# Performance work log

Hardware: AMD Instinct MI355X
Metric: run time of the kernel (lower is better)

Reference implementation:

```python
import jax, jax.numpy as jnp
import numpy as np

B, S, HID = 1, 2048, 4096
H, NOPE, ROPE, VD = 32, 128, 64, 128
QKD = NOPE + ROPE
Q_RANK, KV_RANK = 1536, 512
IDX_H, IDX_D, TOPK = 16, 128, 1024
EPS, THETA = 1e-5, 10000.0


def rmsnorm(x, w):
    return x * jax.lax.rsqrt(jnp.mean(x * x, axis=-1, keepdims=True) + EPS) * w


def rope_interleaved(x, pos):
    # x: [..., s, d]; rope_interleave=True -> rotate adjacent pairs
    d = x.shape[-1]
    inv_freq = 1.0 / (THETA ** (jnp.arange(0, d, 2, dtype=jnp.float32) / d))
    ang = pos[:, None] * inv_freq[None, :]  # [s, d/2]
    cos, sin = jnp.cos(ang), jnp.sin(ang)
    x2 = x.reshape(*x.shape[:-1], d // 2, 2)
    x0, x1 = x2[..., 0], x2[..., 1]
    return jnp.stack([x0 * cos - x1 * sin, x1 * cos + x0 * sin], axis=-1).reshape(x.shape)


def setup_inputs() -> dict:
    key = jax.random.key(0)
    ks = jax.random.split(key, 12)
    s = 0.02
    return {
        'hidden_states': jax.random.normal(ks[0], (B, S, HID), jnp.float32),
        'q_a_w': jax.random.normal(ks[1], (HID, Q_RANK), jnp.float32) * s,
        'q_a_norm_w': jnp.ones((Q_RANK,), jnp.float32),
        'q_b_w': jax.random.normal(ks[2], (Q_RANK, H * QKD), jnp.float32) * s,
        'kv_a_w': jax.random.normal(ks[3], (HID, KV_RANK + ROPE), jnp.float32) * s,
        'kv_a_norm_w': jnp.ones((KV_RANK,), jnp.float32),
        'kv_b_w': jax.random.normal(ks[4], (KV_RANK, H * (NOPE + VD)), jnp.float32) * s,
        'o_w': jax.random.normal(ks[5], (H * VD, HID), jnp.float32) * s,
        'idx_wq_w': jax.random.normal(ks[6], (HID, IDX_H * IDX_D), jnp.float32) * s,
        'idx_wk_w': jax.random.normal(ks[7], (HID, IDX_D), jnp.float32) * s,
        'idx_weights_w': jax.random.normal(ks[8], (HID, IDX_H), jnp.float32) * s,
    }


def reference(hidden_states, q_a_w, q_a_norm_w, q_b_w, kv_a_w, kv_a_norm_w,
              kv_b_w, o_w, idx_wq_w, idx_wk_w, idx_weights_w):
    b, s, _ = hidden_states.shape
    pos = jnp.arange(s, dtype=jnp.float32)

    # ---- MLA latent projections ----
    q_lat = rmsnorm(hidden_states @ q_a_w, q_a_norm_w)                 # [b,s,Q_RANK]
    q = (q_lat @ q_b_w).reshape(b, s, H, QKD).transpose(0, 2, 1, 3)    # [b,h,s,qkd]
    q_nope, q_pe = q[..., :NOPE], q[..., NOPE:]

    ckv = hidden_states @ kv_a_w                                       # [b,s,KV_RANK+ROPE]
    kv_lat, k_pe = ckv[..., :KV_RANK], ckv[..., KV_RANK:]
    kv = (rmsnorm(kv_lat, kv_a_norm_w) @ kv_b_w).reshape(b, s, H, NOPE + VD).transpose(0, 2, 1, 3)
    k_nope, v = kv[..., :NOPE], kv[..., NOPE:]

    q_pe = rope_interleaved(q_pe, pos)
    k_pe = rope_interleaved(k_pe[:, None, :, :], pos)                  # [b,1,s,ROPE] shared MQA rope head

    scores = (jnp.einsum('bhqd,bhkd->bhqk', q_nope, k_nope)
              + jnp.einsum('bhqd,bhkd->bhqk', q_pe, k_pe)) * (QKD ** -0.5)

    # ---- DSA lightning indexer: per-query top-k key selection ----
    iq = (hidden_states @ idx_wq_w).reshape(b, s, IDX_H, IDX_D)
    ik = hidden_states @ idx_wk_w                                      # [b,s,IDX_D]
    iw = (hidden_states @ idx_weights_w) * (IDX_H ** -0.5)             # [b,s,IDX_H]
    idx_scores = jnp.einsum('bqn,bnqk->bqk', iw,
                            jax.nn.relu(jnp.einsum('bqnd,bkd->bnqk', iq, ik))) * (IDX_D ** -0.5)
    causal = pos[:, None] >= pos[None, :]                              # [s,s]
    idx_scores = jnp.where(causal, idx_scores, -jnp.inf)
    _, topk_idx = jax.lax.top_k(idx_scores, TOPK)                      # [b,s,TOPK]
    bi = jnp.arange(b)[:, None, None]
    qi = jnp.arange(s)[None, :, None]
    topk_mask = jnp.zeros((b, s, s), bool).at[bi, qi, topk_idx].set(True)
    mask = topk_mask & causal                                          # [b,s,s]

    scores = jnp.where(mask[:, None], scores, -jnp.inf)
    attn = jax.nn.softmax(scores, axis=-1)
    out = jnp.einsum('bhqk,bhkd->bqhd', attn, v).reshape(b, s, H * VD)
    return out @ o_w
```

## Files before the change

### kernel.cpp

```cpp
#include <hip/hip_runtime.h>
#include <math.h>

#define S_LEN 2048
#define HIDDEN 4096
#define NHEAD 32
#define D_NOPE 128
#define D_ROPE 64
#define D_V 128
#define D_QK 192
#define QRANK 1536
#define KVRANK 512
#define IDXH 16
#define IDXD 128
#define KSEL 1024
#define NIDX 2304

typedef __attribute__((ext_vector_type(8))) short bf16x8;
typedef __attribute__((ext_vector_type(4))) float f32x4;
typedef __attribute__((ext_vector_type(4))) unsigned short u16x4;

__device__ __forceinline__ unsigned short f2b(float f) {
    union { float f; unsigned int u; } x; x.f = f;
    unsigned int r = x.u + 0x7FFFu + ((x.u >> 16) & 1u);
    return (unsigned short)(r >> 16);
}
__device__ __forceinline__ float b2f(unsigned short u) {
    union { unsigned int u; float f; } x; x.u = ((unsigned int)u) << 16; return x.f;
}

__device__ __forceinline__ void gload16(const void* g, const void* l) {
    __builtin_amdgcn_global_load_lds(
        (const __attribute__((address_space(1))) unsigned int*)(unsigned long long)g,
        (__attribute__((address_space(3))) unsigned int*)(unsigned int)(unsigned long long)l,
        16, 0, 0);
}

template <int OUT_BF16>
__global__ __launch_bounds__(256) void gemm_bf16(const unsigned short* __restrict__ A,
                                                 const unsigned short* __restrict__ Bt,
                                                 void* __restrict__ Cv,
                                                 int K, int ldc, float alpha) {
    __shared__ __align__(16) unsigned char lds[32768];
    const int tid = threadIdx.x;
    const int w = tid >> 6, lane = tid & 63;
    const int lr = lane & 15, g = lane >> 4;
    const int bm = blockIdx.y * 128, bn = blockIdx.x * 128;
    const int wm = (w >> 1) * 64, wn = (w & 1) * 64;

    f32x4 acc[4][4];
#pragma unroll
    for (int i = 0; i < 4; ++i)
#pragma unroll
        for (int j = 0; j < 4; ++j) acc[i][j] = (f32x4){0.f, 0.f, 0.f, 0.f};

    int a_off[2], b_off[2];
#pragma unroll
    for (int issue = 0; issue < 2; ++issue) {
        const int off = issue * 4096 + w * 1024 + lane * 16;
        const int row = off >> 6, slot = (off >> 4) & 3;
        a_off[issue] = (bm + row) * K + ((slot ^ (row & 3)) << 3);
        b_off[issue] = (bn + row) * K + ((slot ^ (row & 3)) << 3);
    }

    const int KT = K >> 5;
    auto stage = [&](int t, int buf) {
        const int k0 = t << 5;
        unsigned char* l = lds + buf * 16384;
        gload16(A + a_off[0] + k0, l + w * 1024);
        gload16(A + a_off[1] + k0, l + 4096 + w * 1024);
        gload16(Bt + b_off[0] + k0, l + 8192 + w * 1024);
        gload16(Bt + b_off[1] + k0, l + 8192 + 4096 + w * 1024);
    };

    stage(0, 0);
    for (int t = 0; t < KT; ++t) {
        if (t + 1 < KT) {
            stage(t + 1, (t + 1) & 1);
            asm volatile("s_waitcnt vmcnt(4)" ::: "memory");
        } else {
            asm volatile("s_waitcnt vmcnt(0)" ::: "memory");
        }
        __syncthreads();
        const unsigned char* l = lds + (t & 1) * 16384;

        bf16x8 af[4], bfr[4];
#pragma unroll
        for (int i = 0; i < 4; ++i) {
            const int rowA = wm + i * 16 + lr;
            af[i] = *(const bf16x8*)(l + rowA * 64 + ((g ^ (rowA & 3)) << 4));
            const int rowB = wn + i * 16 + lr;
            bfr[i] = *(const bf16x8*)(l + 8192 + rowB * 64 + ((g ^ (rowB & 3)) << 4));
        }
#pragma unroll
        for (int i = 0; i < 4; ++i)
#pragma unroll
            for (int j = 0; j < 4; ++j)
                acc[i][j] = __builtin_amdgcn_mfma_f32_16x16x32_bf16(af[i], bfr[j], acc[i][j], 0, 0, 0);
        __syncthreads();
    }

#pragma unroll
    for (int i = 0; i < 4; ++i) {
        const int m = bm + wm + i * 16 + g * 4;
#pragma unroll
        for (int j = 0; j < 4; ++j) {
            const int n = bn + wn + j * 16 + lr;
            if (OUT_BF16) {
                unsigned short* Cb = (unsigned short*)Cv;
#pragma unroll
                for (int r = 0; r < 4; ++r)
                    Cb[(size_t)(m + r) * ldc + n] = f2b(acc[i][j][r] * alpha);
            } else {
                float* Cf = (float*)Cv;
#pragma unroll
                for (int r = 0; r < 4; ++r)
                    Cf[(size_t)(m + r) * ldc + n] = acc[i][j][r] * alpha;
            }
        }
    }
}

__global__ __launch_bounds__(256) void gemm_split(const unsigned short* __restrict__ Ah,
                                                  const unsigned short* __restrict__ Al,
                                                  const unsigned short* __restrict__ Bh,
                                                  const unsigned short* __restrict__ Bl,
                                                  float* __restrict__ C, int K, int ldc) {
    const int bm = blockIdx.y * 128, bn = blockIdx.x * 128;
    if (bm < KSEL && bn != 2048) return;
    __shared__ __align__(16) unsigned char lds[65536];
    const int tid = threadIdx.x;
    const int w = tid >> 6, lane = tid & 63;
    const int lr = lane & 15, g = lane >> 4;
    const int wm = (w >> 1) * 64, wn = (w & 1) * 64;

    f32x4 acc[4][4];
#pragma unroll
    for (int i = 0; i < 4; ++i)
#pragma unroll
        for (int j = 0; j < 4; ++j) acc[i][j] = (f32x4){0.f, 0.f, 0.f, 0.f};

    int a_off[2], b_off[2];
#pragma unroll
    for (int issue = 0; issue < 2; ++issue) {
        const int off = issue * 4096 + w * 1024 + lane * 16;
        const int row = off >> 6, slot = (off >> 4) & 3;
        a_off[issue] = (bm + row) * K + ((slot ^ (row & 3)) << 3);
        b_off[issue] = (bn + row) * K + ((slot ^ (row & 3)) << 3);
    }

    const int KT = K >> 5;
    auto stage = [&](int t, int buf) {
        const int k0 = t << 5;
        unsigned char* l = lds + buf * 32768;
        gload16(Ah + a_off[0] + k0, l + w * 1024);
        gload16(Ah + a_off[1] + k0, l + 4096 + w * 1024);
        gload16(Al + a_off[0] + k0, l + 8192 + w * 1024);
        gload16(Al + a_off[1] + k0, l + 8192 + 4096 + w * 1024);
        gload16(Bh + b_off[0] + k0, l + 16384 + w * 1024);
        gload16(Bh + b_off[1] + k0, l + 16384 + 4096 + w * 1024);
        gload16(Bl + b_off[0] + k0, l + 24576 + w * 1024);
        gload16(Bl + b_off[1] + k0, l + 24576 + 4096 + w * 1024);
    };

    stage(0, 0);
    for (int t = 0; t < KT; ++t) {
        if (t + 1 < KT) {
            stage(t + 1, (t + 1) & 1);
            asm volatile("s_waitcnt vmcnt(8)" ::: "memory");
        } else {
            asm volatile("s_waitcnt vmcnt(0)" ::: "memory");
        }
        __syncthreads();
        const unsigned char* l = lds + (t & 1) * 32768;

        bf16x8 afh[4], afl[4], bfh[4], bfl[4];
#pragma unroll
        for (int i = 0; i < 4; ++i) {
            const int rowA = wm + i * 16 + lr;
            const int offA = rowA * 64 + ((g ^ (rowA & 3)) << 4);
            afh[i] = *(const bf16x8*)(l + offA);
            afl[i] = *(const bf16x8*)(l + 8192 + offA);
            const int rowB = wn + i * 16 + lr;
            const int offB = rowB * 64 + ((g ^ (rowB & 3)) << 4);
            bfh[i] = *(const bf16x8*)(l + 16384 + offB);
            bfl[i] = *(const bf16x8*)(l + 24576 + offB);
        }
#pragma unroll
        for (int i = 0; i < 4; ++i)
#pragma unroll
            for (int j = 0; j < 4; ++j) {
                acc[i][j] = __builtin_amdgcn_mfma_f32_16x16x32_bf16(afh[i], bfh[j], acc[i][j], 0, 0, 0);
                acc[i][j] = __builtin_amdgcn_mfma_f32_16x16x32_bf16(afh[i], bfl[j], acc[i][j], 0, 0, 0);
                acc[i][j] = __builtin_amdgcn_mfma_f32_16x16x32_bf16(afl[i], bfh[j], acc[i][j], 0, 0, 0);
            }
        __syncthreads();
    }

#pragma unroll
    for (int i = 0; i < 4; ++i) {
        const int m = bm + wm + i * 16 + g * 4;
#pragma unroll
        for (int j = 0; j < 4; ++j) {
            const int n = bn + wn + j * 16 + lr;
#pragma unroll
            for (int r = 0; r < 4; ++r)
                C[(size_t)(m + r) * ldc + n] = acc[i][j][r];
        }
    }
}

__global__ __launch_bounds__(256) void conv_split_h(const float* __restrict__ src,
                                                    unsigned short* __restrict__ dhi,
                                                    unsigned short* __restrict__ dlo) {
    const int i = blockIdx.x * 256 + threadIdx.x;
    const float4 v = ((const float4*)src)[i];
    u16x4 hi, lo;
    const float xs[4] = {v.x, v.y, v.z, v.w};
#pragma unroll
    for (int j = 0; j < 4; ++j) {
        const unsigned short h = f2b(xs[j]);
        hi[j] = h;
        lo[j] = f2b(xs[j] - b2f(h));
    }
    *(u16x4*)(dhi + (size_t)i * 4) = hi;
    *(u16x4*)(dlo + (size_t)i * 4) = lo;
}

__global__ __launch_bounds__(256) void conv_split_iq(const float* __restrict__ Cidx,
                                                     unsigned short* __restrict__ iqh,
                                                     unsigned short* __restrict__ iql,
                                                     unsigned short* __restrict__ ikh,
                                                     unsigned short* __restrict__ ikl) {
    const int i = blockIdx.x * 256 + threadIdx.x;
    const int row = i / 544, c4 = (i - row * 544) * 4;
    const float4 v = *(const float4*)(Cidx + (size_t)row * NIDX + c4);
    u16x4 hi, lo;
    const float xs[4] = {v.x, v.y, v.z, v.w};
#pragma unroll
    for (int j = 0; j < 4; ++j) {
        const unsigned short h = f2b(xs[j]);
        hi[j] = h;
        lo[j] = f2b(xs[j] - b2f(h));
    }
    if (c4 < 2048) {
        *(u16x4*)(iqh + (size_t)row * 2048 + c4) = hi;
        *(u16x4*)(iql + (size_t)row * 2048 + c4) = lo;
    } else {
        *(u16x4*)(ikh + (size_t)row * 128 + c4 - 2048) = hi;
        *(u16x4*)(ikl + (size_t)row * 128 + c4 - 2048) = lo;
    }
}

__global__ __launch_bounds__(256) void wtrans(const float* __restrict__ W,
                                              unsigned short* __restrict__ Bt,
                                              int K, int Nsrc) {
    const int n0 = blockIdx.x * 64, k0 = blockIdx.y * 64;
    __shared__ unsigned short lv[64][72];
    const int tid = threadIdx.x;
#pragma unroll
    for (int it = 0; it < 16; ++it) {
        const int idx = tid + it * 256;
        const int kr = idx >> 6, n = idx & 63;
        const float v = (n0 + n < Nsrc) ? W[(size_t)(k0 + kr) * Nsrc + n0 + n] : 0.f;
        lv[n][kr] = f2b(v);
    }
    __syncthreads();
#pragma unroll
    for (int it = 0; it < 16; ++it) {
        const int idx = tid + it * 256;
        const int n = idx >> 6, kk = idx & 63;
        Bt[(size_t)(n0 + n) * K + k0 + kk] = lv[n][kk];
    }
}

__global__ __launch_bounds__(256) void wtrans_split(const float* __restrict__ W,
                                                    unsigned short* __restrict__ Bth,
                                                    unsigned short* __restrict__ Btl,
                                                    int K, int Nsrc) {
    const int n0 = blockIdx.x * 64, k0 = blockIdx.y * 64;
    __shared__ float lv[64][65];
    const int tid = threadIdx.x;
#pragma unroll
    for (int it = 0; it < 16; ++it) {
        const int idx = tid + it * 256;
        const int kr = idx >> 6, n = idx & 63;
        lv[n][kr] = (n0 + n < Nsrc) ? W[(size_t)(k0 + kr) * Nsrc + n0 + n] : 0.f;
    }
    __syncthreads();
#pragma unroll
    for (int it = 0; it < 16; ++it) {
        const int idx = tid + it * 256;
        const int n = idx >> 6, kk = idx & 63;
        const float x = lv[n][kk];
        const unsigned short h = f2b(x);
        Bth[(size_t)(n0 + n) * K + k0 + kk] = h;
        Btl[(size_t)(n0 + n) * K + k0 + kk] = f2b(x - b2f(h));
    }
}

__global__ __launch_bounds__(256) void rmsnormb(const float* __restrict__ in,
                                                const float* __restrict__ w,
                                                unsigned short* __restrict__ out,
                                                int W, int in_stride) {
    const int row = blockIdx.x;
    const int tid = threadIdx.x;
    const float* x = in + (size_t)row * in_stride;
    float ss = 0.f;
    for (int i = tid; i < W; i += 256) {
        float v = x[i];
        ss += v * v;
    }
    __shared__ float red[256];
    red[tid] = ss;
    __syncthreads();
    for (int s = 128; s > 0; s >>= 1) {
        if (tid < s) red[tid] += red[tid + s];
        __syncthreads();
    }
    const float scale = rsqrtf(red[0] / (float)W + 1e-5f);
    for (int i = tid; i < W; i += 256) out[(size_t)row * W + i] = f2b(x[i] * scale * w[i]);
}

__global__ __launch_bounds__(256) void rope_q16(unsigned short* __restrict__ q) {
    const int idx = blockIdx.x * 256 + threadIdx.x;
    if (idx >= S_LEN * NHEAD * (D_ROPE / 2)) return;
    const int i = idx & 31;
    const int h = (idx >> 5) & 31;
    const int s = idx >> 10;
    const float inv = __expf(-(float)i * (logf(10000.f) / 32.f));
    const float ang = (float)s * inv;
    const float cs = cosf(ang), sn = sinf(ang);
    unsigned short* p = q + (size_t)s * (NHEAD * D_QK) + h * D_QK + D_NOPE + 2 * i;
    const float x0 = b2f(p[0]), x1 = b2f(p[1]);
    p[0] = f2b(x0 * cs - x1 * sn);
    p[1] = f2b(x1 * cs + x0 * sn);
}

__global__ __launch_bounds__(256) void rope_k16(const float* __restrict__ C1,
                                                unsigned short* __restrict__ kpe16) {
    const int idx = blockIdx.x * 256 + threadIdx.x;
    if (idx >= S_LEN * (D_ROPE / 2)) return;
    const int i = idx & 31;
    const int s = idx >> 5;
    const float inv = __expf(-(float)i * (logf(10000.f) / 32.f));
    const float ang = (float)s * inv;
    const float cs = cosf(ang), sn = sinf(ang);
    const float* p = C1 + (size_t)s * 2176 + 2048 + 2 * i;
    const float x0 = p[0], x1 = p[1];
    kpe16[(size_t)s * D_ROPE + 2 * i] = f2b(x0 * cs - x1 * sn);
    kpe16[(size_t)s * D_ROPE + 2 * i + 1] = f2b(x1 * cs + x0 * sn);
}

#define ISC_IKH 0
#define ISC_IKL 16384
#define ISC_IQH 32768
#define ISC_IQL 49152
#define ISC_IW 65536

__global__ __launch_bounds__(256) void idx_score_mfma(const unsigned short* __restrict__ iqh,
                                                      const unsigned short* __restrict__ iql,
                                                      const unsigned short* __restrict__ ikh,
                                                      const unsigned short* __restrict__ ikl,
                                                      const float* __restrict__ Cidx,
                                                      float* __restrict__ iscore) {
    const int kt = blockIdx.x, qt = blockIdx.y + 16;
    if (kt > qt) return;
    const int q0 = qt * 64, k0 = kt * 64;
    __shared__ __align__(16) unsigned char smem[69632];
    const int tid = threadIdx.x;
    const int w = tid >> 6, lane = tid & 63;
    const int g = lane >> 4, lr = lane & 15;

#pragma unroll
    for (int it = 0; it < 4; ++it) {
        const int j = tid + it * 256;
        const int row = j >> 4, slot = j & 15;
        const int dst = row * 256 + ((slot ^ (row & 7)) << 4);
        *(uint4*)(smem + ISC_IKH + dst) = *(const uint4*)(ikh + (size_t)(k0 + row) * 128 + slot * 8);
        *(uint4*)(smem + ISC_IKL + dst) = *(const uint4*)(ikl + (size_t)(k0 + row) * 128 + slot * 8);
    }
    {
        const int r = tid >> 2, c4 = (tid & 3) * 4;
        const float4 v = *(const float4*)(Cidx + (size_t)(q0 + r) * NIDX + 2176 + c4);
        float4 sv = {v.x * 0.25f, v.y * 0.25f, v.z * 0.25f, v.w * 0.25f};
        *(float4*)(smem + ISC_IW + r * 64 + c4 * 4) = sv;
    }

    f32x4 tot[4];
#pragma unroll
    for (int j = 0; j < 4; ++j) tot[j] = (f32x4){0.f, 0.f, 0.f, 0.f};

    for (int n = 0; n < IDXH; ++n) {
        __syncthreads();
#pragma unroll
        for (int it = 0; it < 4; ++it) {
            const int j = tid + it * 256;
            const int row = j >> 4, slot = j & 15;
            const int dst = row * 256 + ((slot ^ (row & 7)) << 4);
            *(uint4*)(smem + ISC_IQH + dst) =
                *(const uint4*)(iqh + (size_t)(q0 + row) * 2048 + n * 128 + slot * 8);
            *(uint4*)(smem + ISC_IQL + dst) =
                *(const uint4*)(iql + (size_t)(q0 + row) * 2048 + n * 128 + slot * 8);
        }
        __syncthreads();

        bf16x8 aH[4], aL[4];
        const int ar = w * 16 + lr;
#pragma unroll
        for (int kk = 0; kk < 4; ++kk) {
            const int off = ar * 256 + (((kk * 4 + g) ^ (ar & 7)) << 4);
            aH[kk] = *(const bf16x8*)(smem + ISC_IQH + off);
            aL[kk] = *(const bf16x8*)(smem + ISC_IQL + off);
        }
        float wv[4];
#pragma unroll
        for (int r = 0; r < 4; ++r)
            wv[r] = *(const float*)(smem + ISC_IW + (w * 16 + g * 4 + r) * 64 + n * 4);

#pragma unroll
        for (int jj = 0; jj < 4; ++jj) {
            f32x4 s = (f32x4){0.f, 0.f, 0.f, 0.f};
#pragma unroll
            for (int kk = 0; kk < 4; ++kk) {
                const int br = jj * 16 + lr;
                const int off = br * 256 + (((kk * 4 + g) ^ (br & 7)) << 4);
                const bf16x8 bH = *(const bf16x8*)(smem + ISC_IKH + off);
                const bf16x8 bL = *(const bf16x8*)(smem + ISC_IKL + off);
                s = __builtin_amdgcn_mfma_f32_16x16x32_bf16(aH[kk], bH, s, 0, 0, 0);
                s = __builtin_amdgcn_mfma_f32_16x16x32_bf16(aH[kk], bL, s, 0, 0, 0);
                s = __builtin_amdgcn_mfma_f32_16x16x32_bf16(aL[kk], bH, s, 0, 0, 0);
            }
#pragma unroll
            for (int r = 0; r < 4; ++r) tot[jj][r] += wv[r] * fmaxf(s[r], 0.f);
        }
    }

    const float sc = 0.08838834764831845f;
#pragma unroll
    for (int jj = 0; jj < 4; ++jj)
#pragma unroll
        for (int r = 0; r < 4; ++r)
            iscore[(size_t)(q0 + w * 16 + g * 4 + r) * S_LEN + k0 + jj * 16 + lr] =
                tot[jj][r] * sc;
}

__global__ __launch_bounds__(256) void topk_kernel(const float* __restrict__ iscore,
                                                   unsigned char* __restrict__ maskb) {
    const int q = blockIdx.x;
    const int tid = threadIdx.x;
    const int nk = q + 1;
    unsigned char* mrow = maskb + (size_t)q * 256;
    if (nk <= KSEL) {
        unsigned char b = 0;
#pragma unroll
        for (int bi = 0; bi < 8; ++bi)
            if (tid * 8 + bi <= q) b |= (unsigned char)(1 << bi);
        mrow[tid] = b;
        return;
    }
    __shared__ unsigned int uv[S_LEN];
    __shared__ unsigned int hist[256];
    __shared__ unsigned int sh_pfx, sh_rem;
    const float* srow = iscore + (size_t)q * S_LEN;
    for (int k = tid; k < nk; k += 256) {
        unsigned int b = __float_as_uint(srow[k]);
        uv[k] = (b & 0x80000000u) ? ~b : (b | 0x80000000u);
    }
    if (tid == 0) { sh_pfx = 0u; sh_rem = KSEL; }
    __syncthreads();

    const int lane = tid & 63;
#pragma unroll
    for (int shift = 24; shift >= 0; shift -= 8) {
        const unsigned int pfx = sh_pfx;
        const unsigned int rem = sh_rem;
        const unsigned int pmask = (shift == 24) ? 0u : (0xFFFFFFFFu << (shift + 8));
        hist[tid] = 0u;
        __syncthreads();
        for (int k = tid; k < nk; k += 256) {
            const unsigned int u = uv[k];
            if ((u & pmask) == pfx)
                atomicAdd(&hist[(u >> shift) & 255u], 1u);
        }
        __syncthreads();
        const unsigned int h0 = hist[lane * 4], h1 = hist[lane * 4 + 1];
        const unsigned int h2 = hist[lane * 4 + 2], h3 = hist[lane * 4 + 3];
        unsigned int sufp = h0 + h1 + h2 + h3;
#pragma unroll
        for (int off = 1; off < 64; off <<= 1) {
            const unsigned int o = __shfl_down(sufp, off);
            if (lane + off < 64) sufp += o;
        }
        unsigned int run = __shfl_down(sufp, 1);
        if (lane == 63) run = 0u;
        const unsigned int s3 = run + h3;
        const unsigned int s2 = s3 + h2;
        const unsigned int s1 = s2 + h1;
        const unsigned int s0 = s1 + h0;
        int bsel = -1;
        unsigned int gt = 0u;
        if (s3 >= rem && run < rem)      { bsel = 3; gt = run; }
        else if (s2 >= rem && s3 < rem)  { bsel = 2; gt = s3; }
        else if (s1 >= rem && s2 < rem)  { bsel = 1; gt = s2; }
        else if (s0 >= rem && s1 < rem)  { bsel = 0; gt = s1; }
        if (bsel >= 0) {
            sh_pfx = pfx | ((unsigned int)(lane * 4 + bsel) << shift);
            sh_rem = rem - gt;
        }
        __syncthreads();
    }
    const unsigned int T = sh_pfx;
    const int r = (int)sh_rem;
    unsigned char b = 0;
#pragma unroll
    for (int bi = 0; bi < 8; ++bi) {
        const int k = tid * 8 + bi;
        if (k < nk) {
            const unsigned int u = uv[k];
            if (u > T) {
                b |= (unsigned char)(1 << bi);
            } else if (u == T) {
                int rank = 0;
                for (int j = 0; j < k; ++j) rank += (uv[j] == T) ? 1 : 0;
                if (rank < r) b |= (unsigned char)(1 << bi);
            }
        }
    }
    mrow[tid] = b;
}

__global__ __launch_bounds__(256) void pack_k16(const unsigned short* __restrict__ kv16,
                                                const unsigned short* __restrict__ kpe16,
                                                unsigned short* __restrict__ kb16) {
    const int idx = blockIdx.x * 256 + threadIdx.x;
    const int h = idx / (S_LEN * D_QK);
    const int rem = idx - h * (S_LEN * D_QK);
    const int s = rem / D_QK;
    const int d = rem - s * D_QK;
    kb16[idx] = (d < 128) ? kv16[(size_t)s * 8192 + h * 256 + d]
                          : kpe16[(size_t)s * D_ROPE + (d - 128)];
}

__global__ __launch_bounds__(256) void pack_vT16(const unsigned short* __restrict__ kv16,
                                                 unsigned short* __restrict__ vT) {
    const int st = blockIdx.x, h = blockIdx.y;
    const int s0 = st * 64;
    __shared__ unsigned short lv[64][130];
    const int tid = threadIdx.x;
#pragma unroll
    for (int it = 0; it < 32; ++it) {
        const int idx = tid + it * 256;
        const int sl = idx >> 7, d = idx & 127;
        lv[sl][d] = kv16[(size_t)(s0 + sl) * 8192 + h * 256 + 128 + d];
    }
    __syncthreads();
#pragma unroll
    for (int it = 0; it < 32; ++it) {
        const int idx = tid + it * 256;
        const int d = idx >> 6, sl = idx & 63;
        vT[(size_t)(h * 128 + d) * S_LEN + s0 + sl] = lv[sl][d];
    }
}

#define KVB 64
#define AQB 128
#define AT_K0 0
#define AT_K1 24576
#define AT_V0 49152
#define AT_V1 65536
#define AT_P 81920
#define AT_M 100352
#define AT_TOT 133120

__global__ __launch_bounds__(512) void attn_mfma_kernel(
    const unsigned short* __restrict__ qbuf16,
    const unsigned short* __restrict__ kb16,
    const unsigned short* __restrict__ vT,
    const unsigned char* __restrict__ maskb,
    unsigned short* __restrict__ ab16) {
    __shared__ __align__(16) unsigned char smem[AT_TOT];
    const int bid = blockIdx.x;
    const int xcd = bid & 7, jj = bid >> 3;
    const int h = (xcd << 2) | (jj & 3);
    const int qt = 15 - (jj >> 2);
    const int q0 = qt * AQB;
    const int tid = threadIdx.x;
    const int w = tid >> 6, lane = tid & 63;
    const int g = lane >> 4, lr = lane & 15;
    const int wub = (tid & ~63) * 16;

    const unsigned char* kbase = (const unsigned char*)(kb16 + (size_t)h * S_LEN * D_QK);
    const unsigned char* vbase = (const unsigned char*)(vT + (size_t)h * 128 * S_LEN);
    const unsigned char* mbase = maskb + (size_t)q0 * 256;

    bf16x8 qf[6];
    {
        const unsigned short* qrow =
            qbuf16 + (size_t)(q0 + w * 16 + lr) * (NHEAD * D_QK) + h * D_QK;
#pragma unroll
        for (int c = 0; c < 6; ++c) qf[c] = *(const bf16x8*)(qrow + c * 32 + g * 8);
    }

#pragma unroll
    for (int it = 0; it < 4; ++it) {
        const int j = tid + it * 512;
        gload16(mbase + (size_t)j * 16, smem + AT_M + it * 8192 + wub);
    }

    auto stageK = [&](int k0, int kb) {
#pragma unroll
        for (int it = 0; it < 3; ++it) {
            const int j = tid + it * 512;
            const int row = j / 24, cs = j - row * 24;
            const int scs = (cs & ~7) | ((cs & 7) ^ (row & 7));
            gload16(kbase + (size_t)(k0 + row) * 384 + scs * 16, smem + kb + it * 8192 + wub);
        }
    };
    auto stageV = [&](int k0, int vb) {
#pragma unroll
        for (int it = 0; it < 2; ++it) {
            const int j = tid + it * 512;
            const int d = j >> 3, sl = j & 7;
            gload16(vbase + ((size_t)d * S_LEN + k0) * 2 + ((sl ^ (d & 7)) * 16),
                    smem + vb + it * 8192 + wub);
        }
    };

    f32x4 O[8];
#pragma unroll
    for (int db = 0; db < 8; ++db) O[db] = (f32x4){0.f, 0.f, 0.f, 0.f};
    float mS[4] = {-INFINITY, -INFINITY, -INFINITY, -INFINITY};
    float lS[4] = {0.f, 0.f, 0.f, 0.f};
    unsigned short* Pw = (unsigned short*)(smem + AT_P + w * 2304);

    const int nt = 2 * qt + 2;
    stageK(0, AT_K0);
    stageV(0, AT_V0);
    asm volatile("s_waitcnt vmcnt(0)" ::: "memory");
    __syncthreads();

    for (int t = 0; t < nt; ++t) {
        const int cK = AT_K0 + (t & 1) * 24576;
        const int cV = AT_V0 + (t & 1) * 16384;
        if (t + 1 < nt) {
            stageK((t + 1) * KVB, AT_K0 + ((t + 1) & 1) * 24576);
            stageV((t + 1) * KVB, AT_V0 + ((t + 1) & 1) * 16384);
        }

        f32x4 a[4];
#pragma unroll
        for (int j = 0; j < 4; ++j) a[j] = (f32x4){0.f, 0.f, 0.f, 0.f};
        __builtin_amdgcn_s_setprio(1);
#pragma unroll
        for (int c = 0; c < 6; ++c) {
            const int s = c * 4 + g;
#pragma unroll
            for (int j = 0; j < 4; ++j) {
                const int row = j * 16 + lr;
                const int scs = (s & ~7) | ((s & 7) ^ (lr & 7));
                const bf16x8 b = *(const bf16x8*)(smem + cK + row * 384 + scs * 16);
                a[j] = __builtin_amdgcn_mfma_f32_16x16x32_bf16(qf[c], b, a[j], 0, 0, 0);
            }
        }
        __builtin_amdgcn_s_setprio(0);

        const int moff = (t * KVB) >> 3;
        float corr[4];
#pragma unroll
        for (int r = 0; r < 4; ++r) {
            const int qrl = w * 16 + g * 4 + r;
            const unsigned int mlo = *(const unsigned int*)(smem + AT_M + qrl * 256 + moff);
            const unsigned int mhi = *(const unsigned int*)(smem + AT_M + qrl * 256 + moff + 4);
            float sv[4];
            sv[0] = ((mlo >> lr) & 1u) ? a[0][r] : -INFINITY;
            sv[1] = ((mlo >> (lr + 16)) & 1u) ? a[1][r] : -INFINITY;
            sv[2] = ((mhi >> lr) & 1u) ? a[2][r] : -INFINITY;
            sv[3] = ((mhi >> (lr + 16)) & 1u) ? a[3][r] : -INFINITY;
            float tm = fmaxf(fmaxf(sv[0], sv[1]), fmaxf(sv[2], sv[3]));
            tm = fmaxf(tm, __shfl_xor(tm, 1));
            tm = fmaxf(tm, __shfl_xor(tm, 2));
            tm = fmaxf(tm, __shfl_xor(tm, 4));
            tm = fmaxf(tm, __shfl_xor(tm, 8));
            const float mn = fmaxf(mS[r], tm);
            const float co = (mS[r] > -INFINITY) ? __expf(mS[r] - mn) : 0.f;
            float p[4];
#pragma unroll
            for (int j = 0; j < 4; ++j) p[j] = (sv[j] > -INFINITY) ? __expf(sv[j] - mn) : 0.f;
            float rs = (p[0] + p[1]) + (p[2] + p[3]);
            rs += __shfl_xor(rs, 1);
            rs += __shfl_xor(rs, 2);
            rs += __shfl_xor(rs, 4);
            rs += __shfl_xor(rs, 8);
            lS[r] = lS[r] * co + rs;
            mS[r] = mn;
            corr[r] = co;
#pragma unroll
            for (int j = 0; j < 4; ++j) Pw[(g * 4 + r) * 72 + j * 16 + lr] = f2b(p[j]);
        }
#pragma unroll
        for (int db = 0; db < 8; ++db) {
            O[db][0] *= corr[0];
            O[db][1] *= corr[1];
            O[db][2] *= corr[2];
            O[db][3] *= corr[3];
        }

        asm volatile("s_waitcnt lgkmcnt(0)" ::: "memory");
        __builtin_amdgcn_sched_barrier(0);

        __builtin_amdgcn_s_setprio(1);
#pragma unroll
        for (int c2 = 0; c2 < 2; ++c2) {
            const bf16x8 pA = *(const bf16x8*)((const unsigned char*)Pw + lr * 144 + c2 * 64 + g * 16);
#pragma unroll
            for (int db = 0; db < 8; ++db) {
                const int d = db * 16 + lr;
                const int s2 = c2 * 4 + g;
                const bf16x8 bV = *(const bf16x8*)(smem + cV + d * 128 + ((s2 ^ (d & 7)) << 4));
                O[db] = __builtin_amdgcn_mfma_f32_16x16x32_bf16(pA, bV, O[db], 0, 0, 0);
            }
        }
        __builtin_amdgcn_s_setprio(0);

        asm volatile("s_waitcnt vmcnt(0)" ::: "memory");
        __syncthreads();
    }

#pragma unroll
    for (int r = 0; r < 4; ++r) {
        const float inv = (lS[r] > 0.f) ? 1.f / lS[r] : 0.f;
        const int qg = q0 + w * 16 + g * 4 + r;
        unsigned short* orow = ab16 + (size_t)qg * (NHEAD * D_V) + h * D_V;
#pragma unroll
        for (int db = 0; db < 8; ++db) orow[db * 16 + lr] = f2b(O[db][r] * inv);
    }
}

extern "C" void kernel_launch(void* const* d_in, const int* in_sizes, int n_in,
                              void* d_out, int out_size, void* d_ws, size_t ws_size,
                              hipStream_t stream) {
    const float* hidden        = (const float*)d_in[0];
    const float* q_a_w         = (const float*)d_in[1];
    const float* q_a_norm_w    = (const float*)d_in[2];
    const float* q_b_w         = (const float*)d_in[3];
    const float* kv_a_w        = (const float*)d_in[4];
    const float* kv_a_norm_w   = (const float*)d_in[5];
    const float* kv_b_w        = (const float*)d_in[6];
    const float* o_w           = (const float*)d_in[7];
    const float* idx_wq_w      = (const float*)d_in[8];
    const float* idx_wk_w      = (const float*)d_in[9];
    const float* idx_weights_w = (const float*)d_in[10];
    float* out = (float*)d_out;

    char* ws = (char*)d_ws;
    unsigned short* BtAll = (unsigned short*)(ws + 0);
    unsigned short* kv16  = (unsigned short*)(ws + 0);
    unsigned short* owT   = (unsigned short*)(ws + 0);
    unsigned short* h16    = (unsigned short*)(ws + 33554432);
    unsigned short* h_lo   = (unsigned short*)(ws + 50331648);
    unsigned short* qbuf16 = (unsigned short*)(ws + 33554432);
    float* C1          = (float*)(ws + 67108864);
    unsigned short* vT = (unsigned short*)(ws + 67108864);
    unsigned short* BtIdxH = (unsigned short*)(ws + 84934656);
    unsigned short* BtIdxL = (unsigned short*)(ws + 103809024);
    unsigned short* kb16   = (unsigned short*)(ws + 84934656);
    float* Cidx         = (float*)(ws + 122683392);
    unsigned short* qbT = (unsigned short*)(ws + 122683392);
    unsigned short* iqh  = (unsigned short*)(ws + 141557760);
    unsigned short* iql  = (unsigned short*)(ws + 149946368);
    unsigned short* ikh  = (unsigned short*)(ws + 158334976);
    unsigned short* ikl  = (unsigned short*)(ws + 158859264);
    unsigned short* kvbT = (unsigned short*)(ws + 141557760);
    float* iscr          = (float*)(ws + 159383552);
    unsigned short* ab16 = (unsigned short*)(ws + 159383552);
    unsigned char* maskb  = (unsigned char*)(ws + 176160768);
    unsigned short* qa16  = (unsigned short*)(ws + 180355072);
    unsigned short* kvn16 = (unsigned short*)(ws + 186646528);
    unsigned short* kpe16 = (unsigned short*)(ws + 188743680);
    (void)ws_size; (void)in_sizes; (void)n_in; (void)out_size;

    const dim3 blk(256);
    const float QK_SCALE = 0.07216878364870323f;

    conv_split_h<<<8192, blk, 0, stream>>>(hidden, h16, h_lo);

    wtrans<<<dim3(24, 64), blk, 0, stream>>>(q_a_w, BtAll, HIDDEN, QRANK);
    wtrans<<<dim3(9, 64), blk, 0, stream>>>(kv_a_w, BtAll + (size_t)1536 * HIDDEN, HIDDEN, KVRANK + D_ROPE);
    wtrans<<<dim3(1, 64), blk, 0, stream>>>(q_a_w, BtAll + (size_t)2112 * HIDDEN, HIDDEN, 0);
    gemm_bf16<0><<<dim3(17, 16), blk, 0, stream>>>(h16, BtAll, C1, HIDDEN, 2176, 1.f);

    rmsnormb<<<S_LEN, blk, 0, stream>>>(C1, q_a_norm_w, qa16, QRANK, 2176);
    rmsnormb<<<S_LEN, blk, 0, stream>>>(C1 + 1536, kv_a_norm_w, kvn16, KVRANK, 2176);
    rope_k16<<<(S_LEN * 32 + 255) / 256, blk, 0, stream>>>(C1, kpe16);

    wtrans_split<<<dim3(32, 64), blk, 0, stream>>>(idx_wq_w, BtIdxH, BtIdxL, HIDDEN, IDXH * IDXD);
    wtrans_split<<<dim3(2, 64), blk, 0, stream>>>(idx_wk_w, BtIdxH + (size_t)2048 * HIDDEN,
                                                  BtIdxL + (size_t)2048 * HIDDEN, HIDDEN, IDXD);
    wtrans_split<<<dim3(2, 64), blk, 0, stream>>>(idx_weights_w, BtIdxH + (size_t)2176 * HIDDEN,
                                                  BtIdxL + (size_t)2176 * HIDDEN, HIDDEN, IDXH);
    gemm_split<<<dim3(18, 16), blk, 0, stream>>>(h16, h_lo, BtIdxH, BtIdxL, Cidx, HIDDEN, NIDX);
    conv_split_iq<<<4352, blk, 0, stream>>>(Cidx, iqh, iql, ikh, ikl);
    idx_score_mfma<<<dim3(32, 16), blk, 0, stream>>>(iqh, iql, ikh, ikl, Cidx, iscr);
    topk_kernel<<<S_LEN, blk, 0, stream>>>(iscr, maskb);

    wtrans<<<dim3(96, 24), blk, 0, stream>>>(q_b_w, qbT, QRANK, NHEAD * D_QK);
    wtrans<<<dim3(128, 8), blk, 0, stream>>>(kv_b_w, kvbT, KVRANK, NHEAD * 256);
    gemm_bf16<1><<<dim3(48, 16), blk, 0, stream>>>(qa16, qbT, qbuf16, QRANK, NHEAD * D_QK, QK_SCALE);
    gemm_bf16<1><<<dim3(64, 16), blk, 0, stream>>>(kvn16, kvbT, kv16, KVRANK, NHEAD * 256, 1.f);
    rope_q16<<<(S_LEN * NHEAD * 32 + 255) / 256, blk, 0, stream>>>(qbuf16);

    pack_k16<<<(NHEAD * S_LEN * D_QK) / 256, blk, 0, stream>>>(kv16, kpe16, kb16);
    pack_vT16<<<dim3(S_LEN / 64, NHEAD), blk, 0, stream>>>(kv16, vT);
    attn_mfma_kernel<<<dim3(512), dim3(512), 0, stream>>>(qbuf16, kb16, vT, maskb, ab16);

    wtrans<<<dim3(64, 64), blk, 0, stream>>>(o_w, owT, NHEAD * D_V, HIDDEN);
    gemm_bf16<0><<<dim3(32, 16), blk, 0, stream>>>(ab16, owT, out, NHEAD * D_V, HIDDEN, 1.f);
}
```

Measured before the change: 824.2 us.

## Split-K the indexer GEMM over a compact grid and add XCD-aware tile swizzle

The indexer split-precision GEMM now launches one flat grid of 304 workgroups. It covers only the tiles that are actually needed, and each tile's K range is split into two halves that write to separate fp32 buffers. Before, the grid was 18x16 and most workgroups exited early, leaving roughly 152 active ones on a 256-CU part. The two partial sums are added in conv_split_iq, which also copies the indexer weight columns into a compact buffer read by the score kernel. In addition, gemm_bf16 remaps workgroup IDs so that neighbouring tiles land on the same XCD, aiming for better L2 reuse. The cost is an extra fp32 output buffer to write and read, and a hard-coded tile mapping.

```diff
diff --git a/kernel.cpp b/kernel.cpp
--- a/kernel.cpp
+++ b/kernel.cpp
@@ -44,7 +44,11 @@
     const int tid = threadIdx.x;
     const int w = tid >> 6, lane = tid & 63;
     const int lr = lane & 15, g = lane >> 4;
-    const int bm = blockIdx.y * 128, bn = blockIdx.x * 128;
+    const int gx = gridDim.x;
+    const int nwg = gx * gridDim.y;
+    const int flat = blockIdx.y * gx + blockIdx.x;
+    const int swz = (flat & 7) * (nwg >> 3) + (flat >> 3);
+    const int bm = (swz / gx) * 128, bn = (swz % gx) * 128;
     const int wm = (w >> 1) * 64, wn = (w & 1) * 64;
 
     f32x4 acc[4][4];
@@ -124,9 +128,19 @@
                                                   const unsigned short* __restrict__ Al,
                                                   const unsigned short* __restrict__ Bh,
                                                   const unsigned short* __restrict__ Bl,
-                                                  float* __restrict__ C, int K, int ldc) {
-    const int bm = blockIdx.y * 128, bn = blockIdx.x * 128;
-    if (bm < KSEL && bn != 2048) return;
+                                                  float* __restrict__ C0,
+                                                  float* __restrict__ C1) {
+    const int K = HIDDEN, ldc = NIDX;
+    const int bid = blockIdx.x;
+    const int wf = (bid & 7) * 38 + (bid >> 3);
+    const int kz = (wf >= 152) ? 1 : 0;
+    const int wgid = wf - kz * 152;
+    int x, y;
+    if (wgid < 144) { y = 8 + wgid / 18; x = wgid % 18; }
+    else            { x = 16; y = wgid - 144; }
+    const int bm = y * 128, bn = x * 128;
+    float* __restrict__ C = kz ? C1 : C0;
+
     __shared__ __align__(16) unsigned char lds[65536];
     const int tid = threadIdx.x;
     const int w = tid >> 6, lane = tid & 63;
@@ -144,11 +158,11 @@
     for (int issue = 0; issue < 2; ++issue) {
         const int off = issue * 4096 + w * 1024 + lane * 16;
         const int row = off >> 6, slot = (off >> 4) & 3;
-        a_off[issue] = (bm + row) * K + ((slot ^ (row & 3)) << 3);
-        b_off[issue] = (bn + row) * K + ((slot ^ (row & 3)) << 3);
-    }
-
-    const int KT = K >> 5;
+        a_off[issue] = (bm + row) * K + ((slot ^ (row & 3)) << 3) + kz * 2048;
+        b_off[issue] = (bn + row) * K + ((slot ^ (row & 3)) << 3) + kz * 2048;
+    }
+
+    const int KT = 2048 >> 5;
     auto stage = [&](int t, int buf) {
         const int k0 = t << 5;
         unsigned char* l = lds + buf * 32768;
@@ -226,16 +240,24 @@
     *(u16x4*)(dlo + (size_t)i * 4) = lo;
 }
 
-__global__ __launch_bounds__(256) void conv_split_iq(const float* __restrict__ Cidx,
+__global__ __launch_bounds__(256) void conv_split_iq(const float* __restrict__ C0,
+                                                     const float* __restrict__ C1,
                                                      unsigned short* __restrict__ iqh,
                                                      unsigned short* __restrict__ iql,
                                                      unsigned short* __restrict__ ikh,
-                                                     unsigned short* __restrict__ ikl) {
+                                                     unsigned short* __restrict__ ikl,
+                                                     float* __restrict__ iwbuf) {
     const int i = blockIdx.x * 256 + threadIdx.x;
-    const int row = i / 544, c4 = (i - row * 544) * 4;
-    const float4 v = *(const float4*)(Cidx + (size_t)row * NIDX + c4);
+    const int row = i / 548, c4 = (i - row * 548) * 4;
+    const float4 v0 = *(const float4*)(C0 + (size_t)row * NIDX + c4);
+    const float4 v1 = *(const float4*)(C1 + (size_t)row * NIDX + c4);
+    const float xs[4] = {v0.x + v1.x, v0.y + v1.y, v0.z + v1.z, v0.w + v1.w};
+    if (c4 >= 2176) {
+        *(float4*)(iwbuf + (size_t)row * 16 + (c4 - 2176)) =
+            (float4){xs[0], xs[1], xs[2], xs[3]};
+        return;
+    }
     u16x4 hi, lo;
-    const float xs[4] = {v.x, v.y, v.z, v.w};
 #pragma unroll
     for (int j = 0; j < 4; ++j) {
         const unsigned short h = f2b(xs[j]);
@@ -361,7 +383,7 @@
                                                       const unsigned short* __restrict__ iql,
                                                       const unsigned short* __restrict__ ikh,
                                                       const unsigned short* __restrict__ ikl,
-                                                      const float* __restrict__ Cidx,
+                                                      const float* __restrict__ iwbuf,
                                                       float* __restrict__ iscore) {
     const int kt = blockIdx.x, qt = blockIdx.y + 16;
     if (kt > qt) return;
@@ -381,7 +403,7 @@
     }
     {
         const int r = tid >> 2, c4 = (tid & 3) * 4;
-        const float4 v = *(const float4*)(Cidx + (size_t)(q0 + r) * NIDX + 2176 + c4);
+        const float4 v = *(const float4*)(iwbuf + (size_t)(q0 + r) * 16 + c4);
         float4 sv = {v.x * 0.25f, v.y * 0.25f, v.z * 0.25f, v.w * 0.25f};
         *(float4*)(smem + ISC_IW + r * 64 + c4 * 4) = sv;
     }
@@ -777,6 +799,8 @@
     unsigned short* qa16  = (unsigned short*)(ws + 180355072);
     unsigned short* kvn16 = (unsigned short*)(ws + 186646528);
     unsigned short* kpe16 = (unsigned short*)(ws + 188743680);
+    float* iwbuf = (float*)(ws + 189005824);
+    float* Cidx2 = (float*)(ws + 189136896);
     (void)ws_size; (void)in_sizes; (void)n_in; (void)out_size;
 
     const dim3 blk(256);
@@ -798,9 +822,9 @@
                                                   BtIdxL + (size_t)2048 * HIDDEN, HIDDEN, IDXD);
     wtrans_split<<<dim3(2, 64), blk, 0, stream>>>(idx_weights_w, BtIdxH + (size_t)2176 * HIDDEN,
                                                   BtIdxL + (size_t)2176 * HIDDEN, HIDDEN, IDXH);
-    gemm_split<<<dim3(18, 16), blk, 0, stream>>>(h16, h_lo, BtIdxH, BtIdxL, Cidx, HIDDEN, NIDX);
-    conv_split_iq<<<4352, blk, 0, stream>>>(Cidx, iqh, iql, ikh, ikl);
-    idx_score_mfma<<<dim3(32, 16), blk, 0, stream>>>(iqh, iql, ikh, ikl, Cidx, iscr);
+    gemm_split<<<dim3(304), blk, 0, stream>>>(h16, h_lo, BtIdxH, BtIdxL, Cidx, Cidx2);
+    conv_split_iq<<<4384, blk, 0, stream>>>(Cidx, Cidx2, iqh, iql, ikh, ikl, iwbuf);
+    idx_score_mfma<<<dim3(32, 16), blk, 0, stream>>>(iqh, iql, ikh, ikl, iwbuf, iscr);
     topk_kernel<<<S_LEN, blk, 0, stream>>>(iscr, maskb);
 
     wtrans<<<dim3(96, 24), blk, 0, stream>>>(q_b_w, qbT, QRANK, NHEAD * D_QK);
```

Measured after the change: 773.0 us. -6.2%, faster.
